# Kernel tuning notes

Hardware: AMD Instinct MI355X
Metric: run time of the kernel (lower is better)

Reference implementation:

```python
import jax, jax.numpy as jnp
import numpy as np

N = 32768
D = 512          # query_dim = key_dim = value_dim
H = 8            # num_heads


def setup_inputs() -> dict:
    key = jax.random.key(0)
    ks = jax.random.split(key, 8)
    s = 0.02
    return {
        "queries": jax.random.normal(ks[0], (N, D), dtype=jnp.float32),
        "keys": jax.random.normal(ks[1], (N, D), dtype=jnp.float32),
        "values": jax.random.normal(ks[2], (N, D), dtype=jnp.float32),
        # Linear weights stored as [in, out] (torch stores [out, in]; math identical)
        "Wq": jax.random.normal(ks[3], (D, D * H), dtype=jnp.float32) * s,
        "Wk": jax.random.normal(ks[4], (D, D * H), dtype=jnp.float32) * s,
        "Wv": jax.random.normal(ks[5], (D, D * H), dtype=jnp.float32) * s,
        "Wo": jax.random.normal(ks[6], (D * H, D), dtype=jnp.float32) * s,
        "bo": jax.random.normal(ks[7], (D,), dtype=jnp.float32) * s,
    }


def reference(queries, keys, values, Wq, Wk, Wv, Wo, bo):
    # Projections: [N, D] -> [N, H, D]
    Q = (queries @ Wq).reshape(-1, H, D)
    K = (keys @ Wk).reshape(-1, H, D)
    V = (values @ Wv).reshape(-1, H, D)
    # Per-token attention across the HEADS axis (faithful to torch.bmm on [N,H,D])
    attn = jnp.einsum("nhd,ngd->nhg", Q, K)      # [N, H, H], no 1/sqrt(d) scaling
    attn = jax.nn.softmax(attn, axis=-1)
    out = jnp.einsum("nhg,ngd->nhd", attn, V)    # [N, H, D]
    out = out.reshape(-1, H * D)
    return out @ Wo + bo                           # [N, D]
```

## Files before the change

kernel.cpp:

```cpp
#include <hip/hip_runtime.h>
#include <hip/hip_bf16.h>
#include <cstdint>


typedef unsigned short u16;
typedef unsigned int u32;
typedef __bf16 bf16x8 __attribute__((ext_vector_type(8)));
typedef float f32x4 __attribute__((ext_vector_type(4)));

#define DEVI __device__ __forceinline__

DEVI float b2f(u16 u) {
    union { u32 i; float f; } c; c.i = ((u32)u) << 16; return c.f;
}
DEVI u16 f2b(float f) {
    union { float f; u32 i; } c; c.f = f;
    return (u16)((c.i + 0x7FFFu + ((c.i >> 16) & 1u)) >> 16);
}

DEVI void async16(const u16* g, u16* l) {
    __builtin_amdgcn_global_load_lds(
        (const __attribute__((address_space(1))) u32*)g,
        (__attribute__((address_space(3))) u32*)l, 16, 0, 0);
}


__global__ __launch_bounds__(256) void cvt3_bf16(
    const float* __restrict__ a, const float* __restrict__ b,
    const float* __restrict__ c, u16* __restrict__ out, long ostride) {
    const float* in = (blockIdx.z == 0) ? a : (blockIdx.z == 1) ? b : c;
    u16* o = out + (long)blockIdx.z * ostride;
    const int i = blockIdx.x * 256 + threadIdx.x;
    const float4 x = ((const float4*)in)[2 * i];
    const float4 y = ((const float4*)in)[2 * i + 1];
    union { u16 u[8]; uint4 v; } r;
    r.u[0] = f2b(x.x); r.u[1] = f2b(x.y); r.u[2] = f2b(x.z); r.u[3] = f2b(x.w);
    r.u[4] = f2b(y.x); r.u[5] = f2b(y.y); r.u[6] = f2b(y.z); r.u[7] = f2b(y.w);
    ((uint4*)o)[i] = r.v;
}

__global__ void transpose_cvt(const float* __restrict__ in, u16* __restrict__ out,
                              int R, int C) {
    __shared__ float tile[32][33];
    const int c0 = blockIdx.x * 32, r0 = blockIdx.y * 32;
    const int x = threadIdx.x, y = threadIdx.y;
#pragma unroll
    for (int i = 0; i < 4; ++i) {
        const int r = y + i * 8;
        tile[x][r] = in[(long)(r0 + r) * C + c0 + x];
    }
    __syncthreads();
#pragma unroll
    for (int i = 0; i < 4; ++i) {
        const int c = y + i * 8;
        out[(long)(c0 + c) * R + r0 + x] = f2b(tile[c][x]);
    }
}


template <int F32OUT>
__global__ __launch_bounds__(256) void gemm_bt(
    const u16* __restrict__ Ab, const u16* __restrict__ Bb,
    void* __restrict__ Cv, const float* __restrict__ bias,
    int M, int N, int K, long sAz, long sBz, long sCz) {
    __shared__ u16 As[2 * 4096];
    __shared__ u16 Bs[2 * 4096];
    const int tid = threadIdx.x;
    const int wave = tid >> 6, lane = tid & 63;
    const int z = blockIdx.z;
    const u16* A = Ab + (long)z * sAz;
    const u16* BT = Bb + (long)z * sBz;

    int bx, by;
    {
        const int b = blockIdx.y * gridDim.x + blockIdx.x;
        if ((gridDim.x & 7) == 0) {
            const int cb = gridDim.x >> 3;
            const int xcd = b & 7, j = b >> 3;
            bx = xcd * cb + (j % cb);
            by = j / cb;
        } else { bx = blockIdx.x; by = blockIdx.y; }
    }
    const long row0 = (long)by * 128, col0 = (long)bx * 128;
    const int wm = (wave >> 1) * 64, wn = (wave & 1) * 64;
    const int mrow = lane & 15, quad = lane >> 4;

    f32x4 acc[4][4] = {};

    const int srow = lane >> 2;
    const int sg = (lane & 3) ^ ((lane >> 3) & 3);
    const u16* pA = A + (row0 + wave * 32 + srow) * (long)K + sg * 8;
    const u16* pB = BT + (col0 + wave * 32 + srow) * (long)K + sg * 8;
    u16* lA = As + wave * 1024;
    u16* lB = Bs + wave * 1024;
    const long skip = 16 * (long)K;

    async16(pA, lA);
    async16(pA + skip, lA + 512);
    async16(pB, lB);
    async16(pB + skip, lB + 512);

    const int cg = quad ^ ((mrow >> 1) & 3);
    for (int k0 = 0; k0 < K; k0 += 32) {
        const int cur = (k0 >> 5) & 1;
        __syncthreads();
        if (k0 + 32 < K) {
            const int nb = (cur ^ 1) * 4096;
            const long o = k0 + 32;
            async16(pA + o, lA + nb);
            async16(pA + o + skip, lA + nb + 512);
            async16(pB + o, lB + nb);
            async16(pB + o + skip, lB + nb + 512);
        }
        const u16* sA = As + cur * 4096;
        const u16* sB = Bs + cur * 4096;
        bf16x8 af[4], bfr[4];
#pragma unroll
        for (int i = 0; i < 4; ++i)
            af[i] = *(const bf16x8*)(sA + (wm + i * 16 + mrow) * 32 + cg * 8);
#pragma unroll
        for (int j = 0; j < 4; ++j)
            bfr[j] = *(const bf16x8*)(sB + (wn + j * 16 + mrow) * 32 + cg * 8);
#pragma unroll
        for (int i = 0; i < 4; ++i)
#pragma unroll
            for (int j = 0; j < 4; ++j)
                acc[i][j] = __builtin_amdgcn_mfma_f32_16x16x32_bf16(
                    af[i], bfr[j], acc[i][j], 0, 0, 0);
    }

#pragma unroll
    for (int i = 0; i < 4; ++i) {
        const long r = row0 + wm + i * 16 + quad * 4;
#pragma unroll
        for (int j = 0; j < 4; ++j) {
            const long c = col0 + wn + j * 16 + mrow;
            if (F32OUT) {
                float* C = (float*)Cv + (long)z * sCz;
                const float bv = bias[c];
#pragma unroll
                for (int rr = 0; rr < 4; ++rr)
                    C[(r + rr) * (long)N + c] = acc[i][j][rr] + bv;
            } else {
                u16* C = (u16*)Cv + (long)z * sCz;
#pragma unroll
                for (int rr = 0; rr < 4; ++rr)
                    C[(r + rr) * (long)N + c] = f2b(acc[i][j][rr]);
            }
        }
    }
}


__global__ __launch_bounds__(256) void attn_kernel(
    const u16* __restrict__ Qg, const u16* __restrict__ Kg,
    const u16* __restrict__ Vg, u16* __restrict__ Og) {
    __shared__ uint4 sQ[512], sK[512], sV[512];
    __shared__ float part[4][64];
    __shared__ float logitS[64];
    __shared__ float probS[64];
    const int t = threadIdx.x;
    const long base = (long)blockIdx.x * 4096;

    const uint4* q4 = (const uint4*)(Qg + base);
    const uint4* k4 = (const uint4*)(Kg + base);
    const uint4* v4 = (const uint4*)(Vg + base);
    sQ[t] = q4[t]; sQ[t + 256] = q4[t + 256];
    sK[t] = k4[t]; sK[t + 256] = k4[t + 256];
    sV[t] = v4[t]; sV[t + 256] = v4[t + 256];
    __syncthreads();

    const u16* Qs = (const u16*)sQ;
    const u16* Ks = (const u16*)sK;
    const u16* Vs = (const u16*)sV;

    {
        const int pr = t & 63, ch = t >> 6;
        const int h = pr >> 3, g = pr & 7;
        const u16* qp = Qs + h * 512 + ch * 128;
        const u16* kp = Ks + g * 512 + ch * 128;
        float s = 0.f;
#pragma unroll
        for (int i = 0; i < 128; ++i) s += b2f(qp[i]) * b2f(kp[i]);
        part[ch][pr] = s;
    }
    __syncthreads();
    if (t < 64) logitS[t] = part[0][t] + part[1][t] + part[2][t] + part[3][t];
    __syncthreads();
    if (t < 8) {
        float m = logitS[t * 8];
#pragma unroll
        for (int g = 1; g < 8; ++g) m = fmaxf(m, logitS[t * 8 + g]);
        float e[8], sum = 0.f;
#pragma unroll
        for (int g = 0; g < 8; ++g) { e[g] = __expf(logitS[t * 8 + g] - m); sum += e[g]; }
        const float inv = 1.f / sum;
#pragma unroll
        for (int g = 0; g < 8; ++g) probS[t * 8 + g] = e[g] * inv;
    }
    __syncthreads();

    const int hh = t >> 5, d0 = (t & 31) * 16;
    float p[8];
#pragma unroll
    for (int g = 0; g < 8; ++g) p[g] = probS[hh * 8 + g];
    float o[16];
#pragma unroll
    for (int j = 0; j < 16; ++j) o[j] = 0.f;
#pragma unroll
    for (int g = 0; g < 8; ++g) {
        const u16* vp = Vs + g * 512 + d0;
#pragma unroll
        for (int j = 0; j < 16; ++j) o[j] += p[g] * b2f(vp[j]);
    }
    union { u16 u[16]; uint4 v[2]; } ob;
#pragma unroll
    for (int j = 0; j < 16; ++j) ob.u[j] = f2b(o[j]);
    uint4* op = (uint4*)(Og + base + hh * 512 + d0);
    op[0] = ob.v[0]; op[1] = ob.v[1];
}


extern "C" void kernel_launch(void* const* d_in, const int* in_sizes, int n_in,
                              void* d_out, int out_size, void* d_ws, size_t ws_size,
                              hipStream_t stream) {
    const float* Xq = (const float*)d_in[0];
    const float* Xk = (const float*)d_in[1];
    const float* Xv = (const float*)d_in[2];
    const float* Wq = (const float*)d_in[3];
    const float* Wk = (const float*)d_in[4];
    const float* Wv = (const float*)d_in[5];
    const float* Wo = (const float*)d_in[6];
    const float* bo = (const float*)d_in[7];

    const int N = 32768;
    const size_t W = 16777216ull;
    const size_t AO = 268435456ull;

    int McA = 0;
    for (int m = 8192; m >= 1024; m >>= 1)
        if (W + AO + (size_t)m * 27648ull <= ws_size) { McA = m; break; }

    char* ws = (char*)d_ws;
    u16* WqT = (u16*)(ws);
    u16* WoT = (u16*)(ws + 12582912ull);

    dim3 tb(32, 8);
    transpose_cvt<<<dim3(128, 16), tb, 0, stream>>>(Wq, WqT, 512, 4096);
    transpose_cvt<<<dim3(128, 16), tb, 0, stream>>>(Wk, WqT + 2097152, 512, 4096);
    transpose_cvt<<<dim3(128, 16), tb, 0, stream>>>(Wv, WqT + 4194304, 512, 4096);
    transpose_cvt<<<dim3(16, 128), tb, 0, stream>>>(Wo, WoT, 4096, 512);

    if (McA) {
        const int Mc = McA;
        u16* Ao  = (u16*)(ws + W);
        u16* Xb  = (u16*)(ws + W + AO);
        u16* Qc  = Xb + (size_t)3 * Mc * 512;
        u16* Kc  = Qc + (size_t)Mc * 4096;
        u16* Vc  = Kc + (size_t)Mc * 4096;
        const dim3 gProj(32, Mc / 128, 3);
        for (int m0 = 0; m0 < N; m0 += Mc) {
            const long xoff = (long)m0 * 512;
            cvt3_bf16<<<dim3(Mc / 4, 1, 3), 256, 0, stream>>>(
                Xq + xoff, Xk + xoff, Xv + xoff, Xb, (long)Mc * 512);
            gemm_bt<0><<<gProj, 256, 0, stream>>>(Xb, WqT, Qc, nullptr,
                                                  Mc, 4096, 512,
                                                  (long)Mc * 512, 2097152L,
                                                  (long)Mc * 4096);
            attn_kernel<<<Mc, 256, 0, stream>>>(Qc, Kc, Vc, Ao + (long)m0 * 4096);
        }
        gemm_bt<1><<<dim3(4, 256, 1), 256, 0, stream>>>(
            Ao, WoT, d_out, bo, N, 512, 4096, 0L, 0L, 0L);
    } else {
        int Mc = 8192;
        while (Mc > 128 && W + (size_t)Mc * 27648ull > ws_size) Mc >>= 1;
        if (W + (size_t)Mc * 27648ull > ws_size) return;
        u16* Xb = (u16*)(ws + W);
        u16* Qc = Xb + (size_t)3 * Mc * 512;
        u16* Kc = Qc + (size_t)Mc * 4096;
        u16* Vc = Kc + (size_t)Mc * 4096;
        const dim3 gProj(32, Mc / 128, 3);
        const dim3 gOut(4, Mc / 128, 1);
        for (int m0 = 0; m0 < N; m0 += Mc) {
            const long xoff = (long)m0 * 512;
            cvt3_bf16<<<dim3(Mc / 4, 1, 3), 256, 0, stream>>>(
                Xq + xoff, Xk + xoff, Xv + xoff, Xb, (long)Mc * 512);
            gemm_bt<0><<<gProj, 256, 0, stream>>>(Xb, WqT, Qc, nullptr,
                                                  Mc, 4096, 512,
                                                  (long)Mc * 512, 2097152L,
                                                  (long)Mc * 4096);
            attn_kernel<<<Mc, 256, 0, stream>>>(Qc, Kc, Vc, Qc);
            gemm_bt<1><<<gOut, 256, 0, stream>>>(Qc, WoT, (float*)d_out + xoff, bo,
                                                 Mc, 512, 4096, 0L, 0L, 0L);
        }
    }
}
```

Before: 1.391 ms.

## Replace 128x128 GEMM with 256x256 eight-wave pipelined MFMA kernel

```diff
diff --git a/kernel.cpp b/kernel.cpp
--- a/kernel.cpp
+++ b/kernel.cpp
@@ -58,13 +58,68 @@
 }
 
 
+#define VM4 asm volatile("s_waitcnt vmcnt(4)" ::: "memory")
+#define VM0 asm volatile("s_waitcnt vmcnt(0)" ::: "memory")
+#define LGKM0 asm volatile("s_waitcnt lgkmcnt(0)" ::: "memory")
+#define NOOP ((void)0)
+
+#define STAGE_A(t, h)                                                     \
+    do {                                                                  \
+        const u16* _s = pA + (long)(h) * 128 * K + (long)(t) * 64;        \
+        u16* _d = As + (((t) & 1) * 16384) + (h) * 8192 + wave * 512;     \
+        async16(_s, _d);                                                  \
+        async16(_s + 64 * (long)K, _d + 4096);                            \
+    } while (0)
+
+#define STAGE_B(t, h)                                                     \
+    do {                                                                  \
+        const u16* _s = pB + (long)(h) * 128 * K + (long)(t) * 64;        \
+        u16* _d = Bs + (((t) & 1) * 16384) + (h) * 8192 + wave * 512;     \
+        async16(_s, _d);                                                  \
+        async16(_s + 64 * (long)K, _d + 4096);                            \
+    } while (0)
+
+#define PHASE(c, P, STG, VW)                                                   \
+    {                                                                          \
+        const u16* _sA = As + (c) * 16384;                                     \
+        const u16* _sB = Bs + (c) * 16384;                                     \
+        bf16x8 a00 = *(const bf16x8*)(_sA + arow_u + (2 * (P)) * 1024 + s0);   \
+        bf16x8 a01 = *(const bf16x8*)(_sA + arow_u + (2 * (P)) * 1024 + s1);   \
+        bf16x8 a10 = *(const bf16x8*)(_sA + arow_u + (2 * (P) + 1) * 1024 + s0); \
+        bf16x8 a11 = *(const bf16x8*)(_sA + arow_u + (2 * (P) + 1) * 1024 + s1); \
+        if ((P) == 0) {                                                        \
+            _Pragma("unroll") for (int n = 0; n < 4; ++n) {                    \
+                bfr[n][0] = *(const bf16x8*)(_sB + brow_u + n * 1024 + s0);    \
+                bfr[n][1] = *(const bf16x8*)(_sB + brow_u + n * 1024 + s1);    \
+            }                                                                  \
+        }                                                                      \
+        STG;                                                                   \
+        __builtin_amdgcn_s_barrier();                                          \
+        LGKM0;                                                                 \
+        __builtin_amdgcn_s_setprio(1);                                         \
+        _Pragma("unroll") for (int n = 0; n < 4; ++n) {                        \
+            acc[2 * (P)][n] = __builtin_amdgcn_mfma_f32_16x16x32_bf16(         \
+                a00, bfr[n][0], acc[2 * (P)][n], 0, 0, 0);                     \
+            acc[2 * (P)][n] = __builtin_amdgcn_mfma_f32_16x16x32_bf16(         \
+                a01, bfr[n][1], acc[2 * (P)][n], 0, 0, 0);                     \
+            acc[2 * (P) + 1][n] = __builtin_amdgcn_mfma_f32_16x16x32_bf16(     \
+                a10, bfr[n][0], acc[2 * (P) + 1][n], 0, 0, 0);                 \
+            acc[2 * (P) + 1][n] = __builtin_amdgcn_mfma_f32_16x16x32_bf16(     \
+                a11, bfr[n][1], acc[2 * (P) + 1][n], 0, 0, 0);                 \
+        }                                                                      \
+        __builtin_amdgcn_s_setprio(0);                                         \
+        VW;                                                                    \
+        __builtin_amdgcn_s_barrier();                                          \
+    }
+
 template <int F32OUT>
-__global__ __launch_bounds__(256) void gemm_bt(
+__global__ __launch_bounds__(512, 2) void gemm256(
     const u16* __restrict__ Ab, const u16* __restrict__ Bb,
     void* __restrict__ Cv, const float* __restrict__ bias,
     int M, int N, int K, long sAz, long sBz, long sCz) {
-    __shared__ u16 As[2 * 4096];
-    __shared__ u16 Bs[2 * 4096];
+    __shared__ u16 As[2 * 16384];
+    __shared__ u16 Bs[2 * 16384];
+    (void)M;
     const int tid = threadIdx.x;
     const int wave = tid >> 6, lane = tid & 63;
     const int z = blockIdx.z;
@@ -73,83 +128,100 @@
 
     int bx, by;
     {
-        const int b = blockIdx.y * gridDim.x + blockIdx.x;
-        if ((gridDim.x & 7) == 0) {
-            const int cb = gridDim.x >> 3;
-            const int xcd = b & 7, j = b >> 3;
-            bx = xcd * cb + (j % cb);
-            by = j / cb;
+        const int gx = gridDim.x, nwg = gx * gridDim.y;
+        const int b = blockIdx.y * gx + blockIdx.x;
+        if ((nwg & 7) == 0) {
+            const int cpx = nwg >> 3;
+            const int w = (b & 7) * cpx + (b >> 3);
+            bx = w % gx; by = w / gx;
         } else { bx = blockIdx.x; by = blockIdx.y; }
     }
-    const long row0 = (long)by * 128, col0 = (long)bx * 128;
-    const int wm = (wave >> 1) * 64, wn = (wave & 1) * 64;
+    const long row0 = (long)by * 256, col0 = (long)bx * 256;
+
     const int mrow = lane & 15, quad = lane >> 4;
-
-    f32x4 acc[4][4] = {};
-
-    const int srow = lane >> 2;
-    const int sg = (lane & 3) ^ ((lane >> 3) & 3);
-    const u16* pA = A + (row0 + wave * 32 + srow) * (long)K + sg * 8;
-    const u16* pB = BT + (col0 + wave * 32 + srow) * (long)K + sg * 8;
-    u16* lA = As + wave * 1024;
-    u16* lB = Bs + wave * 1024;
-    const long skip = 16 * (long)K;
-
-    async16(pA, lA);
-    async16(pA + skip, lA + 512);
-    async16(pB, lB);
-    async16(pB + skip, lB + 512);
-
-    const int cg = quad ^ ((mrow >> 1) & 3);
-    for (int k0 = 0; k0 < K; k0 += 32) {
-        const int cur = (k0 >> 5) & 1;
-        __syncthreads();
-        if (k0 + 32 < K) {
-            const int nb = (cur ^ 1) * 4096;
-            const long o = k0 + 32;
-            async16(pA + o, lA + nb);
-            async16(pA + o + skip, lA + nb + 512);
-            async16(pB + o, lB + nb);
-            async16(pB + o + skip, lB + nb + 512);
-        }
-        const u16* sA = As + cur * 4096;
-        const u16* sB = Bs + cur * 4096;
-        bf16x8 af[4], bfr[4];
-#pragma unroll
-        for (int i = 0; i < 4; ++i)
-            af[i] = *(const bf16x8*)(sA + (wm + i * 16 + mrow) * 32 + cg * 8);
-#pragma unroll
-        for (int j = 0; j < 4; ++j)
-            bfr[j] = *(const bf16x8*)(sB + (wn + j * 16 + mrow) * 32 + cg * 8);
-#pragma unroll
-        for (int i = 0; i < 4; ++i)
-#pragma unroll
-            for (int j = 0; j < 4; ++j)
-                acc[i][j] = __builtin_amdgcn_mfma_f32_16x16x32_bf16(
-                    af[i], bfr[j], acc[i][j], 0, 0, 0);
-    }
-
-#pragma unroll
-    for (int i = 0; i < 4; ++i) {
-        const long r = row0 + wm + i * 16 + quad * 4;
-#pragma unroll
-        for (int j = 0; j < 4; ++j) {
-            const long c = col0 + wn + j * 16 + mrow;
-            if (F32OUT) {
-                float* C = (float*)Cv + (long)z * sCz;
-                const float bv = bias[c];
+    const int wr = wave >> 2, wc = wave & 3;
+    const int s0 = ((quad ^ (mrow & 7)) << 3);
+    const int s1 = (((4 | quad) ^ (mrow & 7)) << 3);
+    const int arow_u = (wr * 128 + mrow) * 64;
+    const int brow_u = (wc * 64 + mrow) * 64;
+
+    const int sr = tid >> 3;
+    const int skg = ((tid & 7) ^ (sr & 7)) << 3;
+    const u16* pA = A + (row0 + sr) * (long)K + skg;
+    const u16* pB = BT + (col0 + sr) * (long)K + skg;
+
+    f32x4 acc[8][4] = {};
+    bf16x8 bfr[4][2];
+
+    const int NT = K >> 6;
+    const int NI = NT >> 1;
+
+    STAGE_A(0, 0); STAGE_A(0, 1); STAGE_B(0, 0); STAGE_B(0, 1);
+    STAGE_B(1, 0); STAGE_B(1, 1);
+    VM4;
+    __builtin_amdgcn_s_barrier();
+
+#pragma unroll 1
+    for (int it = 0; it < NI - 1; ++it) {
+        const int t1 = 2 * it + 1;
+        PHASE(0, 0, STAGE_A(t1, 0), NOOP);
+        PHASE(0, 1, STAGE_A(t1, 1), NOOP);
+        PHASE(0, 2, STAGE_B(t1 + 1, 0), NOOP);
+        PHASE(0, 3, STAGE_B(t1 + 1, 1), VM4);
+        PHASE(1, 0, STAGE_A(t1 + 1, 0), NOOP);
+        PHASE(1, 1, STAGE_A(t1 + 1, 1), NOOP);
+        PHASE(1, 2, STAGE_B(t1 + 2, 0), NOOP);
+        PHASE(1, 3, STAGE_B(t1 + 2, 1), VM4);
+    }
+    {
+        const int tl = NT - 1;
+        PHASE(0, 0, STAGE_A(tl, 0), NOOP);
+        PHASE(0, 1, STAGE_A(tl, 1), NOOP);
+        PHASE(0, 2, NOOP, NOOP);
+        PHASE(0, 3, NOOP, VM0);
+        PHASE(1, 0, NOOP, NOOP);
+        PHASE(1, 1, NOOP, NOOP);
+        PHASE(1, 2, NOOP, NOOP);
+        PHASE(1, 3, NOOP, NOOP);
+    }
+
+    const long wrow = row0 + wr * 128;
+    const long wcol = col0 + wc * 64;
+    if (F32OUT) {
+        float* C = (float*)Cv + (long)z * sCz;
+        float bv[4];
+#pragma unroll
+        for (int n = 0; n < 4; ++n) bv[n] = bias[wcol + n * 16 + mrow];
+#pragma unroll
+        for (int m = 0; m < 8; ++m) {
+            const long r = wrow + m * 16 + quad * 4;
+#pragma unroll
+            for (int n = 0; n < 4; ++n) {
+                const long c = wcol + n * 16 + mrow;
 #pragma unroll
                 for (int rr = 0; rr < 4; ++rr)
-                    C[(r + rr) * (long)N + c] = acc[i][j][rr] + bv;
-            } else {
-                u16* C = (u16*)Cv + (long)z * sCz;
-#pragma unroll
-                for (int rr = 0; rr < 4; ++rr)
-                    C[(r + rr) * (long)N + c] = f2b(acc[i][j][rr]);
+                    C[(r + rr) * (long)N + c] = acc[m][n][rr] + bv[n];
             }
         }
-    }
-}
+    } else {
+        u16* C = (u16*)Cv + (long)z * sCz;
+#pragma unroll
+        for (int m = 0; m < 8; ++m) {
+            const long r = wrow + m * 16 + quad * 4;
+#pragma unroll
+            for (int n = 0; n < 4; ++n) {
+                const long c = wcol + n * 16 + mrow;
+#pragma unroll
+                for (int rr = 0; rr < 4; ++rr)
+                    C[(r + rr) * (long)N + c] = f2b(acc[m][n][rr]);
+            }
+        }
+    }
+}
+
+#undef PHASE
+#undef STAGE_A
+#undef STAGE_B
 
 
 __global__ __launch_bounds__(256) void attn_kernel(
@@ -258,39 +330,39 @@
         u16* Qc  = Xb + (size_t)3 * Mc * 512;
         u16* Kc  = Qc + (size_t)Mc * 4096;
         u16* Vc  = Kc + (size_t)Mc * 4096;
-        const dim3 gProj(32, Mc / 128, 3);
+        const dim3 gProj(16, Mc / 256, 3);
         for (int m0 = 0; m0 < N; m0 += Mc) {
             const long xoff = (long)m0 * 512;
             cvt3_bf16<<<dim3(Mc / 4, 1, 3), 256, 0, stream>>>(
                 Xq + xoff, Xk + xoff, Xv + xoff, Xb, (long)Mc * 512);
-            gemm_bt<0><<<gProj, 256, 0, stream>>>(Xb, WqT, Qc, nullptr,
+            gemm256<0><<<gProj, 512, 0, stream>>>(Xb, WqT, Qc, nullptr,
                                                   Mc, 4096, 512,
                                                   (long)Mc * 512, 2097152L,
                                                   (long)Mc * 4096);
             attn_kernel<<<Mc, 256, 0, stream>>>(Qc, Kc, Vc, Ao + (long)m0 * 4096);
         }
-        gemm_bt<1><<<dim3(4, 256, 1), 256, 0, stream>>>(
+        gemm256<1><<<dim3(2, 128, 1), 512, 0, stream>>>(
             Ao, WoT, d_out, bo, N, 512, 4096, 0L, 0L, 0L);
     } else {
         int Mc = 8192;
-        while (Mc > 128 && W + (size_t)Mc * 27648ull > ws_size) Mc >>= 1;
+        while (Mc > 256 && W + (size_t)Mc * 27648ull > ws_size) Mc >>= 1;
         if (W + (size_t)Mc * 27648ull > ws_size) return;
         u16* Xb = (u16*)(ws + W);
         u16* Qc = Xb + (size_t)3 * Mc * 512;
         u16* Kc = Qc + (size_t)Mc * 4096;
         u16* Vc = Kc + (size_t)Mc * 4096;
-        const dim3 gProj(32, Mc / 128, 3);
-        const dim3 gOut(4, Mc / 128, 1);
+        const dim3 gProj(16, Mc / 256, 3);
+        const dim3 gOut(2, Mc / 256, 1);
         for (int m0 = 0; m0 < N; m0 += Mc) {
             const long xoff = (long)m0 * 512;
             cvt3_bf16<<<dim3(Mc / 4, 1, 3), 256, 0, stream>>>(
                 Xq + xoff, Xk + xoff, Xv + xoff, Xb, (long)Mc * 512);
-            gemm_bt<0><<<gProj, 256, 0, stream>>>(Xb, WqT, Qc, nullptr,
+            gemm256<0><<<gProj, 512, 0, stream>>>(Xb, WqT, Qc, nullptr,
                                                   Mc, 4096, 512,
                                                   (long)Mc * 512, 2097152L,
                                                   (long)Mc * 4096);
             attn_kernel<<<Mc, 256, 0, stream>>>(Qc, Kc, Vc, Qc);
-            gemm_bt<1><<<gOut, 256, 0, stream>>>(Qc, WoT, (float*)d_out + xoff, bo,
+            gemm256<1><<<gOut, 512, 0, stream>>>(Qc, WoT, (float*)d_out + xoff, bo,
                                                  Mc, 512, 4096, 0L, 0L, 0L);
         }
     }
```

New measurement: 1.426 ms. +2.5%, slower.
